# Kernel tuning notes

Measured on AMD Instinct MI355X. Metric: run time of the kernel, lower is better.

The kernel has to match this reference:

```python
import jax, jax.numpy as jnp
import numpy as np

B, S, H = 2, 4096, 2048          # batch, seq_len, hidden_size
NH, D, W = 8, 128, 4             # num_kv_heads, head_dim, conv_kernel_size (window)
KD = NH * D                      # key_dim == value_dim == 1024
ROPE_BASE = 1000000.0
EPS = 1e-6


def _rope_tables(d, end, base):
    inv = 1.0 / (base ** (np.arange(0, d, 2)[: d // 2].astype(np.float32) / d))
    f = np.outer(np.arange(end, dtype=np.float32), inv)  # [end, d/2]
    return jnp.asarray(np.cos(f)), jnp.asarray(np.sin(f))


def _apply_rope(x, cos, sin):
    # x: [B,S,h,d]; llama-style interleaved pairs (2i, 2i+1)
    x0, x1 = x[..., 0::2], x[..., 1::2]
    c = cos[None, :, None, :]
    s = sin[None, :, None, :]
    o0 = x0 * c - x1 * s
    o1 = x0 * s + x1 * c
    return jnp.stack([o0, o1], axis=-1).reshape(x.shape)


def setup_inputs() -> dict:
    key = jax.random.key(0)
    ks = jax.random.split(key, 7)
    sd = lambda k, shape, fan_in: jax.random.normal(k, shape, jnp.float32) * (fan_in ** -0.5)
    return {
        "x": jax.random.normal(ks[0], (B, S, H), jnp.float32),
        "W_qkv": sd(ks[1], (H, 3 * KD), H),
        "W_z": sd(ks[2], (H, KD), H),
        "W_b": sd(ks[3], (H, NH), H),
        "W_a": sd(ks[4], (H, NH), H),
        "norm_w": jnp.ones((KD,), jnp.float32),
        "W_out": sd(ks[5], (KD, H), KD),
    }


def _forward(x, W_qkv, W_z, W_b, W_a, norm_w, W_out):
    cos, sin = _rope_tables(D, S, ROPE_BASE)
    qkv = x @ W_qkv
    q, k, v = qkv[..., :KD], qkv[..., KD:2 * KD], qkv[..., 2 * KD:]
    z = x @ W_z           # [B,S,KD]
    bg = x @ W_b          # [B,S,NH]
    ag = x @ W_a          # [B,S,NH]

    q4 = _apply_rope(q.reshape(B, S, NH, D), cos, sin)
    k4 = _apply_rope(k.reshape(B, S, NH, D), cos, sin)
    v4 = v.reshape(B, S, NH, D)

    # Windowed gated delta rule: out[i] = sum_{j=i-W..i} (q_i.k_j/sqrt(D)) * sigmoid(a_i*b_j) * v_j
    # Implemented per diagonal offset (W+1 small, fixed) -- never materializes an SxS matrix.
    scale = 1.0 / np.sqrt(D).astype(np.float32)
    out = jnp.zeros_like(v4)
    idx = jnp.arange(S)
    for off in range(W + 1):
        if off == 0:
            kj, vj, bj = k4, v4, bg
        else:
            kj = jnp.pad(k4, ((0, 0), (off, 0), (0, 0), (0, 0)))[:, :S]
            vj = jnp.pad(v4, ((0, 0), (off, 0), (0, 0), (0, 0)))[:, :S]
            bj = jnp.pad(bg, ((0, 0), (off, 0), (0, 0)))[:, :S]
        score = jnp.einsum('bshd,bshd->bsh', q4, kj) * scale
        s = score * jax.nn.sigmoid(ag * bj)
        s = jnp.where((idx >= off)[None, :, None], s, 0.0)
        out = out + s[..., None] * vj
    # position 0 bypasses the attention entirely: output[0] = v[0]
    out = out.at[:, 0].set(v4[:, 0])

    y = out.reshape(B, S, KD) * jax.nn.sigmoid(z)
    # GatedRMSNorm(y, z): rmsnorm(y) * weight * silu(z)
    yf = y.reshape(B * S, KD)
    zf = z.reshape(B * S, KD)
    rms = jnp.sqrt(jnp.mean(yf * yf, axis=-1, keepdims=True) + EPS)
    yn = (yf / rms) * norm_w * (zf * jax.nn.sigmoid(zf))
    return yn.reshape(B, S, KD) @ W_out


def reference(x, W_qkv, W_z, W_b, W_a, norm_w, W_out):
    return _forward(x, W_qkv, W_z, W_b, W_a, norm_w, W_out)
```

## Files before the change

### kernel.cpp

```cpp
#include <hip/hip_runtime.h>
#include <hip/hip_bf16.h>
#include <stdint.h>

#define B_   2
#define S_   4096
#define H_   2048
#define NH_  8
#define D_   128
#define KD_  1024
#define MR   (B_ * S_)
#define NQKVZ 4096

typedef __attribute__((ext_vector_type(8))) short bf16x8;
typedef __attribute__((ext_vector_type(4))) float f32x4;

__device__ __forceinline__ short f2bf(float f) {
    union { float f; uint32_t u; } v; v.f = f;
    uint32_t r = v.u + 0x7FFF + ((v.u >> 16) & 1);
    return (short)(r >> 16);
}
__device__ __forceinline__ float bf2f(unsigned short u) {
    union { uint32_t u; float f; } v; v.u = (uint32_t)u << 16; return v.f;
}

__device__ __forceinline__ void async_ld16(const void* g, void* l) {
    __builtin_amdgcn_global_load_lds(
        (const __attribute__((address_space(1))) uint32_t*)g,
        (__attribute__((address_space(3))) uint32_t*)l, 16, 0, 0);
}

__global__ __launch_bounds__(256) void k_cvt_bgag(const float* __restrict__ x,
                                                  short* __restrict__ xb,
                                                  const float* __restrict__ Wb,
                                                  const float* __restrict__ Wa,
                                                  float* __restrict__ bgag) {
    const int m = blockIdx.x, t = threadIdx.x;
    __shared__ float xs[2048];
    __shared__ float part[256];
    const float4* xr = (const float4*)(x + (size_t)m * H_);
    float4 a = xr[t], b = xr[t + 256];
    ((float4*)xs)[t] = a;
    ((float4*)xs)[t + 256] = b;
    short4 oa, ob;
    oa.x = f2bf(a.x); oa.y = f2bf(a.y); oa.z = f2bf(a.z); oa.w = f2bf(a.w);
    ob.x = f2bf(b.x); ob.y = f2bf(b.y); ob.z = f2bf(b.z); ob.w = f2bf(b.w);
    short4* xo = (short4*)(xb + (size_t)m * H_);
    xo[t] = oa;
    xo[t + 256] = ob;
    __syncthreads();
    int col = t & 15, seg = t >> 4;
    const float* W = (col < 8) ? Wb : Wa;
    int c = col & 7;
    float acc = 0.f;
    int kb = seg * 128;
    for (int k = 0; k < 128; k++) acc += xs[kb + k] * W[(size_t)(kb + k) * 8 + c];
    part[t] = acc;
    __syncthreads();
    if (t < 16) {
        float s = 0.f;
        for (int j = 0; j < 16; j++) s += part[j * 16 + t];
        bgag[(size_t)m * 16 + t] = s;
    }
}

__global__ __launch_bounds__(256) void k_transpose_cvt(const float* __restrict__ W,
                                                       short* __restrict__ Wt,
                                                       int K, int N) {
    __shared__ float tile[32][33];
    int n0 = blockIdx.x * 32, k0 = blockIdx.y * 32;
    int tx = threadIdx.x, ty = threadIdx.y;
#pragma unroll
    for (int i = 0; i < 32; i += 8)
        tile[ty + i][tx] = W[(size_t)(k0 + ty + i) * N + n0 + tx];
    __syncthreads();
#pragma unroll
    for (int i = 0; i < 32; i += 8)
        Wt[(size_t)(n0 + ty + i) * K + k0 + tx] = f2bf(tile[tx][ty + i]);
}

__global__ __launch_bounds__(256) void k_ropetab(float2* __restrict__ ctab) {
    int idx = blockIdx.x * 256 + threadIdx.x;
    int i = idx & 63, s = idx >> 6;
    float inv = exp2f(-(float)i * (2.0f / 128.0f) * 19.931568569324174f);
    float f = (float)s * inv;
    float sn, cs;
    sincosf(f, &sn, &cs);
    ctab[idx] = make_float2(cs, sn);
}

#define PHASE_TAIL() \
    __builtin_amdgcn_s_setprio(0); \
    asm volatile("s_waitcnt vmcnt(%0)" :: "n"(2 + LB) : "memory"); \
    asm volatile("s_barrier" ::: "memory")
#define LDB_P(SET, BASE, KH) \
    _Pragma("unroll") for (int j = 0; j < NF; j++) \
        bf##SET[j] = *(const bf16x8*)((BASE) + 2 * AHB + (KH) * BHB + (wn + j * 16 + mrow) * 64 + kcA)
#define LDA03_P(SET, BASE, KH) \
    _Pragma("unroll") for (int i = 0; i < 4; i++) \
        af##SET[i] = *(const bf16x8*)((BASE) + (KH) * AHB + (wm + i * 16 + mrow) * 64 + kcA)
#define LDA47_S(BASE, KH) \
    _Pragma("unroll") for (int i = 0; i < 4; i++) \
        afS[i] = *(const bf16x8*)((BASE) + (KH) * AHB + (wm + 64 + i * 16 + mrow) * 64 + kcA)
#define MFMA_PH(SET) \
    _Pragma("unroll") for (int i = 0; i < 4; i++) \
    _Pragma("unroll") for (int j = 0; j < NF; j++) \
        acc[i][j] = __builtin_amdgcn_mfma_f32_16x16x32_bf16(af##SET[i], bf##SET[j], acc[i][j], 0, 0, 0); \
    _Pragma("unroll") for (int i = 0; i < 4; i++) \
    _Pragma("unroll") for (int j = 0; j < NF; j++) \
        acc[4 + i][j] = __builtin_amdgcn_mfma_f32_16x16x32_bf16(afS[i], bf##SET[j], acc[4 + i][j], 0, 0, 0)

template <int BN, int EPI>
__global__ __launch_bounds__(512, 2) void k_gemm256(const short* __restrict__ A,
                                                    const short* __restrict__ Bt,
                                                    float* __restrict__ Cf,
                                                    unsigned short* __restrict__ Cb,
                                                    const float2* __restrict__ ctab,
                                                    int M, int N, int K) {
    constexpr int BM = 256;
    constexpr int NF = BN / 64;
    constexpr int LB = BN / 128;
    constexpr int AHB = BM * 64;
    constexpr int BHB = BN * 64;
    constexpr int BUFB = 2 * AHB + 2 * BHB;
    __shared__ __align__(16) char lds[2 * BUFB];

    const int t = threadIdx.x;
    const int lane = t & 63, wave = t >> 6;
    const int mrow = lane & 15;
    const int kcA = (((lane >> 4) ^ ((mrow >> 1) & 3)) * 16);

    const int nwg = gridDim.x;
    const int w0 = blockIdx.x;
    const int wg = (w0 & 7) * (nwg >> 3) + (w0 >> 3);
    const int NB = N / BN;
    const int bn = (wg % NB) * BN;
    const int bm = (wg / NB) * BM;

    const int wm = (wave >> 2) * 128;
    const int wn = (wave & 3) * (BN / 4);

    const short* __restrict__ Ab = A + (size_t)bm * K;
    const short* __restrict__ Bb = Bt + (size_t)bn * K;

    int aoff[2], adst[2];
#pragma unroll
    for (int l = 0; l < 2; l++) {
        int c = t + l * 512;
        int row = c >> 2;
        int kcg = (c & 3) ^ ((row >> 1) & 3);
        aoff[l] = row * K + kcg * 8;
        adst[l] = c * 16;
    }
    int boff[LB], bdst[LB];
#pragma unroll
    for (int l = 0; l < LB; l++) {
        int c = t + l * 512;
        int row = c >> 2;
        int kcg = (c & 3) ^ ((row >> 1) & 3);
        boff[l] = row * K + kcg * 8;
        bdst[l] = c * 16;
    }

    const int NT = K >> 6;

    auto stageA = [&](int kt, int kh, int p) {
        const short* g = Ab + kt * 64 + kh * 32;
        char* d = lds + p * BUFB + kh * AHB;
#pragma unroll
        for (int l = 0; l < 2; l++) async_ld16(g + aoff[l], d + adst[l]);
    };
    auto stageB = [&](int kt, int kh, int p) {
        const short* g = Bb + kt * 64 + kh * 32;
        char* d = lds + p * BUFB + 2 * AHB + kh * BHB;
#pragma unroll
        for (int l = 0; l < LB; l++) async_ld16(g + boff[l], d + bdst[l]);
    };

    f32x4 acc[8][NF] = {};
    bf16x8 afE[4], bfE[NF], afO[4], bfO[NF], afS[4];

    stageA(0, 0, 0); stageB(0, 0, 0);
    stageA(0, 1, 0); stageB(0, 1, 0);
    {
        int k1 = (NT > 1) ? 1 : 0;
        stageA(k1, 0, 1); stageB(k1, 0, 1);
    }
    asm volatile("s_waitcnt vmcnt(%0)" :: "n"(2 * (2 + LB)) : "memory");
    asm volatile("s_barrier" ::: "memory");
    LDB_P(E, lds, 0); LDA03_P(E, lds, 0);
    asm volatile("s_waitcnt vmcnt(%0)" :: "n"(2 + LB) : "memory");
    asm volatile("s_barrier" ::: "memory");

    for (int kt = 0; kt < NT; kt++) {
        const int p = kt & 1;
        const char* base = lds + p * BUFB;
        const char* baseN = lds + (p ^ 1) * BUFB;
        const int k1 = (kt + 1 < NT) ? (kt + 1) : (NT - 1);
        const int k2 = (kt + 2 < NT) ? (kt + 2) : (NT - 1);

        LDA47_S(base, 0);
        LDB_P(O, base, 1); LDA03_P(O, base, 1);
        stageA(k1, 1, p ^ 1); stageB(k1, 1, p ^ 1);
        __builtin_amdgcn_sched_barrier(0);
        __builtin_amdgcn_s_setprio(1);
        MFMA_PH(E);
        PHASE_TAIL();

        LDA47_S(base, 1);
        LDB_P(E, baseN, 0); LDA03_P(E, baseN, 0);
        stageA(k2, 0, p); stageB(k2, 0, p);
        __builtin_amdgcn_sched_barrier(0);
        __builtin_amdgcn_s_setprio(1);
        MFMA_PH(O);
        PHASE_TAIL();
    }
    asm volatile("s_waitcnt vmcnt(0)" ::: "memory");

    const int crow = (lane >> 4) * 4, ccol = lane & 15;
#pragma unroll
    for (int i = 0; i < 8; i++)
#pragma unroll
        for (int j = 0; j < NF; j++) {
            const int col = bn + wn + j * 16 + ccol;
            const int rowb = bm + wm + i * 16 + crow;
            size_t basec = (size_t)rowb * N + col;
            if (EPI == 0) {
#pragma unroll
                for (int r = 0; r < 4; r++)
                    Cf[basec + (size_t)r * N] = acc[i][j][r];
            } else {
                const bool qk = col < 2048;
                const int fi = (col & 127) >> 1;
                const bool even = (col & 1) == 0;
                uint32_t* Cd = (uint32_t*)(Cb + ((size_t)rowb * N + (col & ~1)));
#pragma unroll
                for (int r = 0; r < 4; r++) {
                    float v = acc[i][j][r];
                    if (qk) {
                        int s = (rowb + r) & (S_ - 1);
                        float2 cs = ctab[s * 64 + fi];
                        float pp = __shfl_xor(v, 1);
                        v = even ? v * cs.x - pp * cs.y : v * cs.x + pp * cs.y;
                    }
                    int hb = (int)(unsigned short)f2bf(v);
                    int pb = __shfl_xor(hb, 1);
                    if (even)
                        Cd[(size_t)r * (N >> 1)] = (uint32_t)(hb | (pb << 16));
                }
            }
        }
}

__global__ __launch_bounds__(256) void k_attn(const unsigned short* __restrict__ qkvz,
                                              const float* __restrict__ bgag,
                                              const float* __restrict__ norm_w,
                                              short* __restrict__ yn) {
    const int m = blockIdx.x;
    const int s = m & (S_ - 1);
    const int t = threadIdx.x;
    __shared__ unsigned short kvls[5][2048];
    __shared__ unsigned short qzls[2048];
    __shared__ float sc[NH_][5];
    __shared__ float red[4];
    const int nOff = (s < 4 ? s : 4) + 1;

    for (int off = 0; off < 5; off++) {
        if (off < nOff) {
            const ushort4* r = (const ushort4*)(qkvz + (size_t)(m - off) * NQKVZ + 1024);
            ushort4* d = (ushort4*)kvls[off];
            d[t] = r[t];
            d[t + 256] = r[t + 256];
        }
    }
    {
        const unsigned short* r = qkvz + (size_t)m * NQKVZ;
        ushort4* d = (ushort4*)qzls;
        d[t] = ((const ushort4*)r)[t];
        d[256 + t] = ((const ushort4*)(r + 3072))[t];
    }
    __syncthreads();

    {
        const int h = t >> 5, l = t & 31;
        float qv[4];
#pragma unroll
        for (int d = 0; d < 4; d++) qv[d] = bf2f(qzls[h * 128 + l * 4 + d]);
        const float ag = bgag[(size_t)m * 16 + 8 + h];
#pragma unroll
        for (int off = 0; off < 5; off++) {
            float acc = 0.f;
            if (off < nOff) {
#pragma unroll
                for (int d = 0; d < 4; d++)
                    acc += qv[d] * bf2f(kvls[off][h * 128 + l * 4 + d]);
            }
#pragma unroll
            for (int w = 1; w < 32; w <<= 1) acc += __shfl_xor(acc, w);
            if (l == 0) {
                float val = 0.f;
                if (off < nOff) {
                    float bg = bgag[(size_t)(m - off) * 16 + h];
                    float g = 1.f / (1.f + expf(-ag * bg));
                    val = acc * 0.08838834764831845f * g;
                }
                sc[h][off] = val;
            }
        }
    }
    __syncthreads();

    const int e0 = t * 4, h = e0 >> 7;
    float o[4] = {0.f, 0.f, 0.f, 0.f};
    if (s == 0) {
#pragma unroll
        for (int d = 0; d < 4; d++) o[d] = bf2f(kvls[0][1024 + e0 + d]);
    } else {
        for (int off = 0; off < nOff; off++) {
            float w = sc[h][off];
#pragma unroll
            for (int d = 0; d < 4; d++) o[d] += w * bf2f(kvls[off][1024 + e0 + d]);
        }
    }
    float y[4], zs4[4], ss = 0.f;
#pragma unroll
    for (int d = 0; d < 4; d++) {
        float z = bf2f(qzls[1024 + e0 + d]);
        float sg = 1.f / (1.f + expf(-z));
        y[d] = o[d] * sg;
        zs4[d] = z * sg;
        ss += y[d] * y[d];
    }
    const int wave = t >> 6, lane = t & 63;
#pragma unroll
    for (int w = 1; w < 64; w <<= 1) ss += __shfl_xor(ss, w);
    if (lane == 0) red[wave] = ss;
    __syncthreads();
    float tot = red[0] + red[1] + red[2] + red[3];
    float rinv = 1.f / sqrtf(tot * (1.0f / 1024.0f) + 1e-6f);
    short4 ov;
    ov.x = f2bf(y[0] * rinv * norm_w[e0 + 0] * zs4[0]);
    ov.y = f2bf(y[1] * rinv * norm_w[e0 + 1] * zs4[1]);
    ov.z = f2bf(y[2] * rinv * norm_w[e0 + 2] * zs4[2]);
    ov.w = f2bf(y[3] * rinv * norm_w[e0 + 3] * zs4[3]);
    ((short4*)yn)[(size_t)m * 256 + t] = ov;
}

extern "C" void kernel_launch(void* const* d_in, const int* in_sizes, int n_in,
                              void* d_out, int out_size, void* d_ws, size_t ws_size,
                              hipStream_t stream) {
    const float* x      = (const float*)d_in[0];
    const float* W_qkv  = (const float*)d_in[1];
    const float* W_z    = (const float*)d_in[2];
    const float* W_b    = (const float*)d_in[3];
    const float* W_a    = (const float*)d_in[4];
    const float* norm_w = (const float*)d_in[5];
    const float* W_out  = (const float*)d_in[6];
    float* out = (float*)d_out;

    char* ws = (char*)d_ws;
    short* xb    = (short*)ws;          ws += (size_t)MR * H_ * 2;
    short* Wt1   = (short*)ws;          ws += (size_t)NQKVZ * H_ * 2;
    short* Wt2   = (short*)ws;          ws += (size_t)H_ * KD_ * 2;
    unsigned short* qkvzb = (unsigned short*)ws; ws += (size_t)MR * NQKVZ * 2;
    float* bgag  = (float*)ws;          ws += (size_t)MR * 16 * 4;
    short* yn    = (short*)ws;          ws += (size_t)MR * KD_ * 2;
    float2* ctab = (float2*)ws;         ws += (size_t)S_ * 64 * 8;

    k_cvt_bgag<<<MR, 256, 0, stream>>>(x, xb, W_b, W_a, bgag);
    k_transpose_cvt<<<dim3(3072 / 32, 2048 / 32), dim3(32, 8), 0, stream>>>(W_qkv, Wt1, 2048, 3072);
    k_transpose_cvt<<<dim3(1024 / 32, 2048 / 32), dim3(32, 8), 0, stream>>>(W_z, Wt1 + (size_t)3072 * 2048, 2048, 1024);
    k_transpose_cvt<<<dim3(2048 / 32, 1024 / 32), dim3(32, 8), 0, stream>>>(W_out, Wt2, 1024, 2048);
    k_ropetab<<<S_ * 64 / 256, 256, 0, stream>>>(ctab);
    k_gemm256<256, 1><<<(MR / 256) * (NQKVZ / 256), 512, 0, stream>>>(
        xb, Wt1, nullptr, qkvzb, ctab, MR, NQKVZ, H_);
    k_attn<<<MR, 256, 0, stream>>>(qkvzb, bgag, norm_w, yn);
    k_gemm256<256, 0><<<(MR / 256) * (H_ / 256), 512, 0, stream>>>(
        yn, Wt2, out, nullptr, nullptr, MR, H_, KD_);
}
```

Measured before the change: 471.0 us.

## Coalesce output GEMM stores via LDS and batch bg/ag projection rows

The fp32 output GEMM epilogue now writes accumulators into padded LDS and then emits coalesced float4 row stores, replacing scattered scalar stores. The bg/ag projection kernel processes four rows per block against a pre-transposed W_b/W_a, giving contiguous vectorized weight reads that are reused across rows. A small extra transpose kernel and a larger LDS buffer are added, and the extra syncs could cost occupancy.

```diff
diff --git a/kernel.cpp b/kernel.cpp
--- a/kernel.cpp
+++ b/kernel.cpp
@@ -29,37 +29,61 @@
         (__attribute__((address_space(3))) uint32_t*)l, 16, 0, 0);
 }
 
-__global__ __launch_bounds__(256) void k_cvt_bgag(const float* __restrict__ x,
-                                                  short* __restrict__ xb,
-                                                  const float* __restrict__ Wb,
-                                                  const float* __restrict__ Wa,
-                                                  float* __restrict__ bgag) {
-    const int m = blockIdx.x, t = threadIdx.x;
-    __shared__ float xs[2048];
-    __shared__ float part[256];
-    const float4* xr = (const float4*)(x + (size_t)m * H_);
-    float4 a = xr[t], b = xr[t + 256];
-    ((float4*)xs)[t] = a;
-    ((float4*)xs)[t + 256] = b;
-    short4 oa, ob;
-    oa.x = f2bf(a.x); oa.y = f2bf(a.y); oa.z = f2bf(a.z); oa.w = f2bf(a.w);
-    ob.x = f2bf(b.x); ob.y = f2bf(b.y); ob.z = f2bf(b.z); ob.w = f2bf(b.w);
-    short4* xo = (short4*)(xb + (size_t)m * H_);
-    xo[t] = oa;
-    xo[t + 256] = ob;
-    __syncthreads();
-    int col = t & 15, seg = t >> 4;
-    const float* W = (col < 8) ? Wb : Wa;
-    int c = col & 7;
-    float acc = 0.f;
-    int kb = seg * 128;
-    for (int k = 0; k < 128; k++) acc += xs[kb + k] * W[(size_t)(kb + k) * 8 + c];
-    part[t] = acc;
-    __syncthreads();
-    if (t < 16) {
+__global__ __launch_bounds__(256) void k_wba(const float* __restrict__ Wb,
+                                             const float* __restrict__ Wa,
+                                             float* __restrict__ Wba) {
+    int idx = blockIdx.x * 256 + threadIdx.x;
+    int k = idx & 2047, c = idx >> 11;
+    float v = (c < 8) ? Wb[(size_t)k * 8 + c] : Wa[(size_t)k * 8 + (c - 8)];
+    Wba[(size_t)c * 2048 + k] = v;
+}
+
+__global__ __launch_bounds__(256) void k_cvt_bgag4(const float* __restrict__ x,
+                                                   short* __restrict__ xb,
+                                                   const float* __restrict__ Wba,
+                                                   float* __restrict__ bgag) {
+    const int m0 = blockIdx.x * 4, t = threadIdx.x;
+    __shared__ float xs[4][2048];
+    __shared__ float part[4][256];
+#pragma unroll
+    for (int rr = 0; rr < 4; rr++) {
+        const float4* xr = (const float4*)(x + (size_t)(m0 + rr) * H_);
+        float4 a = xr[t], b = xr[t + 256];
+        ((float4*)xs[rr])[t] = a;
+        ((float4*)xs[rr])[t + 256] = b;
+        short4 oa, ob;
+        oa.x = f2bf(a.x); oa.y = f2bf(a.y); oa.z = f2bf(a.z); oa.w = f2bf(a.w);
+        ob.x = f2bf(b.x); ob.y = f2bf(b.y); ob.z = f2bf(b.z); ob.w = f2bf(b.w);
+        short4* xo = (short4*)(xb + (size_t)(m0 + rr) * H_);
+        xo[t] = oa;
+        xo[t + 256] = ob;
+    }
+    __syncthreads();
+    const int c = t & 15, seg = t >> 4;
+    const int kb = seg * 128;
+    const float4* W4 = (const float4*)(Wba + (size_t)c * 2048 + kb);
+    const float4* x0 = (const float4*)&xs[0][kb];
+    const float4* x1 = (const float4*)&xs[1][kb];
+    const float4* x2 = (const float4*)&xs[2][kb];
+    const float4* x3 = (const float4*)&xs[3][kb];
+    float a0 = 0.f, a1 = 0.f, a2 = 0.f, a3 = 0.f;
+#pragma unroll 8
+    for (int k4 = 0; k4 < 32; k4++) {
+        float4 w = W4[k4];
+        float4 v0 = x0[k4], v1 = x1[k4], v2 = x2[k4], v3 = x3[k4];
+        a0 += w.x * v0.x + w.y * v0.y + w.z * v0.z + w.w * v0.w;
+        a1 += w.x * v1.x + w.y * v1.y + w.z * v1.z + w.w * v1.w;
+        a2 += w.x * v2.x + w.y * v2.y + w.z * v2.z + w.w * v2.w;
+        a3 += w.x * v3.x + w.y * v3.y + w.z * v3.z + w.w * v3.w;
+    }
+    part[0][t] = a0; part[1][t] = a1; part[2][t] = a2; part[3][t] = a3;
+    __syncthreads();
+    if (t < 64) {
+        int rr = t >> 4, cc = t & 15;
         float s = 0.f;
-        for (int j = 0; j < 16; j++) s += part[j * 16 + t];
-        bgag[(size_t)m * 16 + t] = s;
+#pragma unroll
+        for (int j = 0; j < 16; j++) s += part[rr][j * 16 + cc];
+        bgag[(size_t)(m0 + rr) * 16 + cc] = s;
     }
 }
 
@@ -122,7 +146,8 @@
     constexpr int AHB = BM * 64;
     constexpr int BHB = BN * 64;
     constexpr int BUFB = 2 * AHB + 2 * BHB;
-    __shared__ __align__(16) char lds[2 * BUFB];
+    constexpr int LDSB = (EPI == 0) ? 133120 : 2 * BUFB;
+    __shared__ __align__(16) char lds[LDSB];
 
     const int t = threadIdx.x;
     const int lane = t & 63, wave = t >> 6;
@@ -217,18 +242,40 @@
     asm volatile("s_waitcnt vmcnt(0)" ::: "memory");
 
     const int crow = (lane >> 4) * 4, ccol = lane & 15;
-#pragma unroll
-    for (int i = 0; i < 8; i++)
-#pragma unroll
-        for (int j = 0; j < NF; j++) {
-            const int col = bn + wn + j * 16 + ccol;
-            const int rowb = bm + wm + i * 16 + crow;
-            size_t basec = (size_t)rowb * N + col;
-            if (EPI == 0) {
-#pragma unroll
-                for (int r = 0; r < 4; r++)
-                    Cf[basec + (size_t)r * N] = acc[i][j][r];
-            } else {
+    if (EPI == 0) {
+        float* lf = (float*)lds;
+#pragma unroll
+        for (int p2 = 0; p2 < 2; p2++) {
+            __syncthreads();
+#pragma unroll
+            for (int i = 0; i < 4; i++) {
+                const int ii = p2 * 4 + i;
+#pragma unroll
+                for (int j = 0; j < NF; j++)
+#pragma unroll
+                    for (int r = 0; r < 4; r++) {
+                        int rl = wm + ii * 16 + crow + r;
+                        int slot = (rl & 63) | ((rl >> 7) << 6);
+                        lf[slot * 260 + wn + j * 16 + ccol] = acc[ii][j][r];
+                    }
+            }
+            __syncthreads();
+#pragma unroll
+            for (int rep = 0; rep < 16; rep++) {
+                int idx = rep * 512 + t;
+                int slot = idx >> 6, c4 = idx & 63;
+                int rl = (slot & 63) + p2 * 64 + ((slot >> 6) << 7);
+                float4 v = *(const float4*)&lf[slot * 260 + c4 * 4];
+                *(float4*)(Cf + (size_t)(bm + rl) * N + bn + c4 * 4) = v;
+            }
+        }
+    } else {
+#pragma unroll
+        for (int i = 0; i < 8; i++)
+#pragma unroll
+            for (int j = 0; j < NF; j++) {
+                const int col = bn + wn + j * 16 + ccol;
+                const int rowb = bm + wm + i * 16 + crow;
                 const bool qk = col < 2048;
                 const int fi = (col & 127) >> 1;
                 const bool even = (col & 1) == 0;
@@ -248,7 +295,7 @@
                         Cd[(size_t)r * (N >> 1)] = (uint32_t)(hb | (pb << 16));
                 }
             }
-        }
+    }
 }
 
 __global__ __launch_bounds__(256) void k_attn(const unsigned short* __restrict__ qkvz,
@@ -365,8 +412,10 @@
     float* bgag  = (float*)ws;          ws += (size_t)MR * 16 * 4;
     short* yn    = (short*)ws;          ws += (size_t)MR * KD_ * 2;
     float2* ctab = (float2*)ws;         ws += (size_t)S_ * 64 * 8;
-
-    k_cvt_bgag<<<MR, 256, 0, stream>>>(x, xb, W_b, W_a, bgag);
+    float* Wba   = (float*)ws;          ws += (size_t)16 * 2048 * 4;
+
+    k_wba<<<16 * 2048 / 256, 256, 0, stream>>>(W_b, W_a, Wba);
+    k_cvt_bgag4<<<MR / 4, 256, 0, stream>>>(x, xb, Wba, bgag);
     k_transpose_cvt<<<dim3(3072 / 32, 2048 / 32), dim3(32, 8), 0, stream>>>(W_qkv, Wt1, 2048, 3072);
     k_transpose_cvt<<<dim3(1024 / 32, 2048 / 32), dim3(32, 8), 0, stream>>>(W_z, Wt1 + (size_t)3072 * 2048, 2048, 1024);
     k_transpose_cvt<<<dim3(2048 / 32, 1024 / 32), dim3(32, 8), 0, stream>>>(W_out, Wt2, 1024, 2048);
```

Result: faster. 450.9 us (-4.3%).
